# Optimization experiments

Measured on AMD Instinct MI355X. Metric: run time of the kernel, lower is better.

Reference implementation:

```python
import jax, jax.numpy as jnp
import numpy as np

B, C, T = 256, 1, 16384   # batch, input_channels, seq_len
H = C                      # hidden_size == input_channels in this module
OUT = 1                    # output_channels


def setup_inputs() -> dict:
    key = jax.random.key(0)
    ks = jax.random.split(key, 11)
    # PyTorch GRU/Linear init: uniform(-1/sqrt(H), 1/sqrt(H)); H=1 -> (-1, 1)
    u = lambda k, shape, s=1.0: jax.random.uniform(k, shape, jnp.float32, -s, s)
    s_lin = 1.0 / np.sqrt(2 * H).astype(np.float32)
    return {
        "x": jax.random.normal(ks[0], (B, C, T), jnp.float32),
        # layer 0: input size C, per direction [3H, C] / [3H, H] / [3H]
        "w_ih0": u(ks[1], (2, 3 * H, C)),
        "w_hh0": u(ks[2], (2, 3 * H, H)),
        "b_ih0": u(ks[3], (2, 3 * H)),
        "b_hh0": u(ks[4], (2, 3 * H)),
        # layers 1-2: input size 2H (bidirectional concat)
        "w_ih12": u(ks[5], (2, 2, 3 * H, 2 * H)),
        "w_hh12": u(ks[6], (2, 2, 3 * H, H)),
        "b_ih12": u(ks[7], (2, 2, 3 * H)),
        "b_hh12": u(ks[8], (2, 2, 3 * H)),
        # output projection Linear(2H -> OUT)
        "w_out": u(ks[9], (OUT, 2 * H), s_lin),
        "b_out": u(ks[10], (OUT,), s_lin),
    }


def _gru_dir(xs, w_ih, w_hh, b_ih, b_hh, reverse):
    """One GRU direction. xs: [T, B, in] -> ys: [T, B, H] (time-aligned)."""
    h0 = jnp.zeros((xs.shape[1], w_hh.shape[1]), xs.dtype)

    def step(h, x_t):
        gi = x_t @ w_ih.T + b_ih          # [B, 3H]
        gh = h @ w_hh.T + b_hh            # [B, 3H]
        ir, iz, inn = jnp.split(gi, 3, axis=-1)
        hr, hz, hn = jnp.split(gh, 3, axis=-1)
        r = jax.nn.sigmoid(ir + hr)
        z = jax.nn.sigmoid(iz + hz)
        n = jnp.tanh(inn + r * hn)
        h_new = (1.0 - z) * n + z * h
        return h_new, h_new

    _, ys = jax.lax.scan(step, h0, xs, reverse=reverse)
    return ys


def _bidir(xs, w_ih_f, w_hh_f, b_ih_f, b_hh_f, w_ih_b, w_hh_b, b_ih_b, b_hh_b):
    fwd = _gru_dir(xs, w_ih_f, w_hh_f, b_ih_f, b_hh_f, reverse=False)
    bwd = _gru_dir(xs, w_ih_b, w_hh_b, b_ih_b, b_hh_b, reverse=True)
    return jnp.concatenate([fwd, bwd], axis=-1)  # [T, B, 2H]


def reference(x, w_ih0, w_hh0, b_ih0, b_hh0, w_ih12, w_hh12, b_ih12, b_hh12, w_out, b_out):
    xs = jnp.transpose(x, (2, 0, 1))  # [B, C, T] -> [T, B, C]
    xs = _bidir(xs, w_ih0[0], w_hh0[0], b_ih0[0], b_hh0[0],
                w_ih0[1], w_hh0[1], b_ih0[1], b_hh0[1])
    for l in range(2):  # GRU layers 1 and 2 (structurally distinct weights)
        xs = _bidir(xs, w_ih12[l, 0], w_hh12[l, 0], b_ih12[l, 0], b_hh12[l, 0],
                    w_ih12[l, 1], w_hh12[l, 1], b_ih12[l, 1], b_hh12[l, 1])
    y = xs @ w_out.T + b_out          # [T, B, OUT]
    return jnp.transpose(y, (1, 2, 0))  # [B, OUT, T]
```

## Files before the change

kernel.cpp:

```cpp
#include <hip/hip_runtime.h>
#include <hip/hip_fp16.h>

#define T_LEN 16384
#define B_SZ  256
#define S_CH  256
#define CL    (T_LEN / S_CH)
#define HALO  32
#define SC    16

__device__ __forceinline__ float ex2(float x)  { return __builtin_amdgcn_exp2f(x); }
__device__ __forceinline__ float rcpf(float x) { return __builtin_amdgcn_rcpf(x); }

__device__ __forceinline__ float ld_cvt(const float* p)  { return *p; }
__device__ __forceinline__ float ld_cvt(const __half* p) { return __half2float(*p); }
__device__ __forceinline__ void  st_cvt(float* p, float v)  { *p = v; }
__device__ __forceinline__ void  st_cvt(__half* p, float v) { *p = __float2half_rn(v); }

__device__ __forceinline__ float gru_step(float h, float preR, float preZ, float preN,
                                          float UR, float UZ, float UN2, float DN2)
{
    float er  = ex2(fmaf(h, UR, preR));
    float ez  = ex2(fmaf(h, UZ, preZ));
    float r   = rcpf(1.0f + er);
    float z   = rcpf(1.0f + ez);
    float hn2 = fmaf(h, UN2, DN2);
    float en  = ex2(fmaf(r, hn2, preN));
    float n   = fmaf(-2.0f, rcpf(1.0f + en), 1.0f);
    float omz = 1.0f - z;
    float zh  = z * h;
    return fmaf(n, omz, zh);
}

template<bool REV>
__device__ void scan0(const float* __restrict__ x,
                      const float* __restrict__ wih, const float* __restrict__ whh,
                      const float* __restrict__ bih, const float* __restrict__ bhh,
                      __half* __restrict__ out, int b, int s)
{
    const int d = REV ? 1 : 0;
    const float L2E = 1.4426950408889634f;
    const float WR  = -L2E * wih[d*3+0];
    const float WZ  = -L2E * wih[d*3+1];
    const float WN  =  2.0f*L2E * wih[d*3+2];
    const float UR  = -L2E * whh[d*3+0];
    const float UZ  = -L2E * whh[d*3+1];
    const float UN2 =  2.0f*L2E * whh[d*3+2];
    const float CR  = -L2E * (bih[d*3+0] + bhh[d*3+0]);
    const float CZ  = -L2E * (bih[d*3+1] + bhh[d*3+1]);
    const float CN  =  2.0f*L2E * bih[d*3+2];
    const float DN2 =  2.0f*L2E * bhh[d*3+2];

    const int warm   = min(HALO, REV ? (T_LEN - (s + 1) * CL) : (s * CL));
    const int nsteps = warm + CL;
    const int t0     = REV ? ((s + 1) * CL - 1 + warm) : (s * CL - warm);

    const float* row = x + (size_t)b * T_LEN;
    __half* po = out + (REV ? B_SZ : 0) + b;

    float xA[SC], xB[SC];
    float h = 0.0f;

    auto LD = [&](float* F, int base) {
        const float4* p = (const float4*)(row + (REV ? (t0 - base - 15) : (t0 + base)));
        float4 v0 = p[0], v1 = p[1], v2 = p[2], v3 = p[3];
        float lin[16] = { v0.x,v0.y,v0.z,v0.w, v1.x,v1.y,v1.z,v1.w,
                          v2.x,v2.y,v2.z,v2.w, v3.x,v3.y,v3.z,v3.w };
        #pragma unroll
        for (int k = 0; k < 16; ++k) F[k] = REV ? lin[15 - k] : lin[k];
        __builtin_amdgcn_sched_barrier(0);
    };

    auto CS = [&](float* F, int base) {
        float ov[SC];
        #pragma unroll
        for (int k = 0; k < SC; ++k) {
            float xv = F[k];
            h = gru_step(h, fmaf(xv, WR, CR), fmaf(xv, WZ, CZ), fmaf(xv, WN, CN),
                         UR, UZ, UN2, DN2);
            ov[k] = h;
        }
        if (base >= warm) {
            #pragma unroll
            for (int k = 0; k < SC; ++k) {
                int t = REV ? (t0 - (base + k)) : (t0 + (base + k));
                st_cvt(po + t * (2 * B_SZ), ov[k]);
            }
        }
    };

    LD(xA, 0);
    const int nsup = nsteps / SC;
    for (int i = 0; i < nsup; i += 2) {
        LD(xB, min((i + 1) * SC, nsteps - SC));
        CS(xA, i * SC);
        LD(xA, min((i + 2) * SC, nsteps - SC));
        CS(xB, (i + 1) * SC);
    }
}

template<bool REV, typename TIN, typename TOUT>
__device__ void scan12(const TIN* __restrict__ in,
                       const float* __restrict__ wih, const float* __restrict__ whh,
                       const float* __restrict__ bih, const float* __restrict__ bhh,
                       TOUT* __restrict__ out, int b, int s)
{
    const int d = REV ? 1 : 0;
    const float L2E = 1.4426950408889634f;
    const float WR0 = -L2E * wih[(d*3+0)*2+0], WR1 = -L2E * wih[(d*3+0)*2+1];
    const float WZ0 = -L2E * wih[(d*3+1)*2+0], WZ1 = -L2E * wih[(d*3+1)*2+1];
    const float WN0 =  2.0f*L2E * wih[(d*3+2)*2+0], WN1 = 2.0f*L2E * wih[(d*3+2)*2+1];
    const float UR  = -L2E * whh[d*3+0];
    const float UZ  = -L2E * whh[d*3+1];
    const float UN2 =  2.0f*L2E * whh[d*3+2];
    const float CR  = -L2E * (bih[d*3+0] + bhh[d*3+0]);
    const float CZ  = -L2E * (bih[d*3+1] + bhh[d*3+1]);
    const float CN  =  2.0f*L2E * bih[d*3+2];
    const float DN2 =  2.0f*L2E * bhh[d*3+2];

    const int warm   = min(HALO, REV ? (T_LEN - (s + 1) * CL) : (s * CL));
    const int nsteps = warm + CL;
    const int t0     = REV ? ((s + 1) * CL - 1 + warm) : (s * CL - warm);

    const TIN* pf = in + b;
    const TIN* pg = in + B_SZ + b;
    TOUT* po = out + (REV ? B_SZ : 0) + b;

    float fA[SC], gA[SC], fB[SC], gB[SC];
    float h = 0.0f;

#define LD12(F, G, base_) { int base = (base_); \
    _Pragma("unroll") for (int k = 0; k < SC; ++k) { \
      int t = REV ? (t0 - (base + k)) : (t0 + (base + k)); \
      F[k] = ld_cvt(pf + t * (2 * B_SZ)); G[k] = ld_cvt(pg + t * (2 * B_SZ)); } \
    __builtin_amdgcn_sched_barrier(0); }

#define CS12(F, G, base_) { int base = (base_); float ov[SC]; \
    _Pragma("unroll") for (int k = 0; k < SC; ++k) { \
      float a = F[k], c = G[k]; \
      float pr = fmaf(a, WR0, fmaf(c, WR1, CR)); \
      float pz = fmaf(a, WZ0, fmaf(c, WZ1, CZ)); \
      float pn = fmaf(a, WN0, fmaf(c, WN1, CN)); \
      h = gru_step(h, pr, pz, pn, UR, UZ, UN2, DN2); ov[k] = h; } \
    if (base >= warm) { \
      _Pragma("unroll") for (int k = 0; k < SC; ++k) { \
        int t = REV ? (t0 - (base + k)) : (t0 + (base + k)); \
        st_cvt(po + t * (2 * B_SZ), ov[k]); } } }

    LD12(fA, gA, 0);
    const int nsup = nsteps / SC;
    for (int i = 0; i < nsup; i += 2) {
        LD12(fB, gB, min((i + 1) * SC, nsteps - SC));
        CS12(fA, gA, i * SC);
        LD12(fA, gA, min((i + 2) * SC, nsteps - SC));
        CS12(fB, gB, (i + 1) * SC);
    }
#undef LD12
#undef CS12
}

__device__ __forceinline__ void decode_blk(int blk, int tid, int& b, int& s, int& dir)
{
    int xcd = blk & 7;
    int j   = blk >> 3;
    int sl  = j & 31;
    int bg  = (j >> 5) & 3;
    dir     = j >> 7;
    s       = xcd * 32 + sl;
    b       = bg * 64 + tid;
}

__global__ void __launch_bounds__(64) k_scan0g(const float* __restrict__ x,
                                               const float* __restrict__ wih,
                                               const float* __restrict__ whh,
                                               const float* __restrict__ bih,
                                               const float* __restrict__ bhh,
                                               __half* __restrict__ out)
{
    int b, s, dir;
    decode_blk(blockIdx.x, threadIdx.x, b, s, dir);
    if (dir == 0) scan0<false>(x, wih, whh, bih, bhh, out, b, s);
    else          scan0<true >(x, wih, whh, bih, bhh, out, b, s);
}

__global__ void __launch_bounds__(64) k_scan1g(const __half* __restrict__ in,
                                               const float* __restrict__ wih,
                                               const float* __restrict__ whh,
                                               const float* __restrict__ bih,
                                               const float* __restrict__ bhh,
                                               __half* __restrict__ out)
{
    int b, s, dir;
    decode_blk(blockIdx.x, threadIdx.x, b, s, dir);
    if (dir == 0) scan12<false>(in, wih, whh, bih, bhh, out, b, s);
    else          scan12<true >(in, wih, whh, bih, bhh, out, b, s);
}

__global__ void __launch_bounds__(64) k_scan2g(const __half* __restrict__ in,
                                               const float* __restrict__ wih,
                                               const float* __restrict__ whh,
                                               const float* __restrict__ bih,
                                               const float* __restrict__ bhh,
                                               float* __restrict__ out)
{
    int b, s, dir;
    decode_blk(blockIdx.x, threadIdx.x, b, s, dir);
    if (dir == 0) scan12<false>(in, wih, whh, bih, bhh, out, b, s);
    else          scan12<true >(in, wih, whh, bih, bhh, out, b, s);
}

__global__ void __launch_bounds__(256) k_proj(const float* __restrict__ h2,
                                              const float* __restrict__ wo,
                                              const float* __restrict__ bo,
                                              float* __restrict__ y)
{
    __shared__ float tile[64][65];
    const int b0 = (blockIdx.x & 3) * 64;
    const int t0 = (blockIdx.x >> 2) * 64;
    const float wf = wo[0], wb = wo[1], bias = bo[0];
    const int bl = threadIdx.x & 63;
    const int tg = threadIdx.x >> 6;
    #pragma unroll
    for (int i = 0; i < 16; ++i) {
        int tl = tg * 16 + i;
        int t  = t0 + tl;
        float f = h2[(size_t)t * (2 * B_SZ) + b0 + bl];
        float g = h2[(size_t)t * (2 * B_SZ) + B_SZ + b0 + bl];
        tile[bl][tl] = fmaf(wf, f, fmaf(wb, g, bias));
    }
    __syncthreads();
    const int c4 = threadIdx.x & 15;
    const int r  = threadIdx.x >> 4;
    #pragma unroll
    for (int i = 0; i < 4; ++i) {
        int brow = r + 16 * i;
        float4 v = make_float4(tile[brow][c4*4+0], tile[brow][c4*4+1],
                               tile[brow][c4*4+2], tile[brow][c4*4+3]);
        ((float4*)y)[(size_t)(b0 + brow) * (T_LEN / 4) + t0 / 4 + c4] = v;
    }
}

extern "C" void kernel_launch(void* const* d_in, const int* in_sizes, int n_in,
                              void* d_out, int out_size, void* d_ws, size_t ws_size,
                              hipStream_t stream)
{
    (void)in_sizes; (void)n_in; (void)out_size; (void)ws_size;
    const float* x      = (const float*)d_in[0];
    const float* w_ih0  = (const float*)d_in[1];
    const float* w_hh0  = (const float*)d_in[2];
    const float* b_ih0  = (const float*)d_in[3];
    const float* b_hh0  = (const float*)d_in[4];
    const float* w_ih12 = (const float*)d_in[5];
    const float* w_hh12 = (const float*)d_in[6];
    const float* b_ih12 = (const float*)d_in[7];
    const float* b_hh12 = (const float*)d_in[8];
    const float* w_out  = (const float*)d_in[9];
    const float* b_out  = (const float*)d_in[10];
    float* y = (float*)d_out;

    char* ws = (char*)d_ws;
    const size_t NN = (size_t)2 * B_SZ * T_LEN;
    __half* l0out = (__half*)ws;
    __half* l1out = (__half*)(ws + NN * 2);
    float*  l2out = (float*)(ws + NN * 4);

    const int nblk = 8 * S_CH;
    k_scan0g<<<nblk, 64, 0, stream>>>(x,     w_ih0,       w_hh0,      b_ih0,      b_hh0,      l0out);
    k_scan1g<<<nblk, 64, 0, stream>>>(l0out, w_ih12 + 0,  w_hh12 + 0, b_ih12 + 0, b_hh12 + 0, l1out);
    k_scan2g<<<nblk, 64, 0, stream>>>(l1out, w_ih12 + 12, w_hh12 + 6, b_ih12 + 6, b_hh12 + 6, l2out);
    k_proj  <<<1024, 256, 0, stream>>>(l2out, w_out, b_out, y);
}
```

Measured before the change: 136.5 us.

## Fuse last GRU layer's two directions with output projection in one kernel

```diff
diff --git a/kernel.cpp b/kernel.cpp
--- a/kernel.cpp
+++ b/kernel.cpp
@@ -98,11 +98,11 @@
     }
 }
 
-template<bool REV, typename TIN, typename TOUT>
-__device__ void scan12(const TIN* __restrict__ in,
-                       const float* __restrict__ wih, const float* __restrict__ whh,
-                       const float* __restrict__ bih, const float* __restrict__ bhh,
-                       TOUT* __restrict__ out, int b, int s)
+template<bool REV>
+__device__ void scan1(const __half* __restrict__ in,
+                      const float* __restrict__ wih, const float* __restrict__ whh,
+                      const float* __restrict__ bih, const float* __restrict__ bhh,
+                      __half* __restrict__ out, int b, int s)
 {
     const int d = REV ? 1 : 0;
     const float L2E = 1.4426950408889634f;
@@ -121,9 +121,9 @@
     const int nsteps = warm + CL;
     const int t0     = REV ? ((s + 1) * CL - 1 + warm) : (s * CL - warm);
 
-    const TIN* pf = in + b;
-    const TIN* pg = in + B_SZ + b;
-    TOUT* po = out + (REV ? B_SZ : 0) + b;
+    const __half* pf = in + b;
+    const __half* pg = in + B_SZ + b;
+    __half* po = out + (REV ? B_SZ : 0) + b;
 
     float fA[SC], gA[SC], fB[SC], gB[SC];
     float h = 0.0f;
@@ -158,6 +158,129 @@
 #undef CS12
 }
 
+template<bool S0, bool SLAST>
+__device__ void scan2p(const __half* __restrict__ in,
+                       const float* __restrict__ wih, const float* __restrict__ whh,
+                       const float* __restrict__ bih, const float* __restrict__ bhh,
+                       const float* __restrict__ wo,  const float* __restrict__ bo,
+                       float* __restrict__ y, int b, int s)
+{
+    const float L2E = 1.4426950408889634f;
+    const float WR0f = -L2E*wih[0], WR1f = -L2E*wih[1];
+    const float WZ0f = -L2E*wih[2], WZ1f = -L2E*wih[3];
+    const float WN0f = 2.0f*L2E*wih[4], WN1f = 2.0f*L2E*wih[5];
+    const float URf  = -L2E*whh[0], UZf = -L2E*whh[1], UN2f = 2.0f*L2E*whh[2];
+    const float CRf  = -L2E*(bih[0]+bhh[0]), CZf = -L2E*(bih[1]+bhh[1]);
+    const float CNf  = 2.0f*L2E*bih[2], DN2f = 2.0f*L2E*bhh[2];
+    const float WR0b = -L2E*wih[6],  WR1b = -L2E*wih[7];
+    const float WZ0b = -L2E*wih[8],  WZ1b = -L2E*wih[9];
+    const float WN0b = 2.0f*L2E*wih[10], WN1b = 2.0f*L2E*wih[11];
+    const float URb  = -L2E*whh[3], UZb = -L2E*whh[4], UN2b = 2.0f*L2E*whh[5];
+    const float CRb  = -L2E*(bih[3]+bhh[3]), CZb = -L2E*(bih[4]+bhh[4]);
+    const float CNb  = 2.0f*L2E*bih[5], DN2b = 2.0f*L2E*bhh[5];
+    const float wf = wo[0], wbk = wo[1], bias = bo[0];
+
+    const __half* pf = in + b;
+    const __half* pg = in + B_SZ + b;
+
+    float fA[SC], gA[SC], fB[SC], gB[SC];
+    float hf[CL];
+    float h;
+
+    constexpr int warmf = S0 ? 0 : HALO;
+    const int t0f = s * CL - warmf;
+
+#define LDF(F, G, base) { \
+    _Pragma("unroll") for (int k = 0; k < SC; ++k) { \
+      int t = t0f + (base) + k; \
+      F[k] = __half2float(pf[t * (2 * B_SZ)]); G[k] = __half2float(pg[t * (2 * B_SZ)]); } \
+    __builtin_amdgcn_sched_barrier(0); }
+#define STEPF(F, G, k) { float a = F[k], c = G[k]; \
+    float pr = fmaf(a, WR0f, fmaf(c, WR1f, CRf)); \
+    float pz = fmaf(a, WZ0f, fmaf(c, WZ1f, CZf)); \
+    float pn = fmaf(a, WN0f, fmaf(c, WN1f, CNf)); \
+    h = gru_step(h, pr, pz, pn, URf, UZf, UN2f, DN2f); }
+#define CSF_B(F, G) { _Pragma("unroll") for (int k = 0; k < SC; ++k) { STEPF(F, G, k); } }
+#define CSF_S(F, G, off) { _Pragma("unroll") for (int k = 0; k < SC; ++k) { STEPF(F, G, k); hf[(off)+k] = h; } }
+
+    h = 0.0f;
+    LDF(fA, gA, 0);
+    LDF(fB, gB, 16);
+    if constexpr (!S0) {
+        CSF_B(fA, gA);
+        LDF(fA, gA, 32);
+        CSF_B(fB, gB);
+        LDF(fB, gB, 48);
+        CSF_S(fA, gA, 0);
+        LDF(fA, gA, 64);
+        CSF_S(fB, gB, 16);
+        LDF(fB, gB, 80);
+        CSF_S(fA, gA, 32);
+        CSF_S(fB, gB, 48);
+    } else {
+        CSF_S(fA, gA, 0);
+        LDF(fA, gA, 32);
+        CSF_S(fB, gB, 16);
+        LDF(fB, gB, 48);
+        CSF_S(fA, gA, 32);
+        CSF_S(fB, gB, 48);
+    }
+#undef LDF
+#undef STEPF
+#undef CSF_B
+#undef CSF_S
+
+    constexpr int warmb = SLAST ? 0 : HALO;
+    const int t0b = (s + 1) * CL - 1 + warmb;
+    float yv[CL];
+
+#define LDB(F, G, base) { \
+    _Pragma("unroll") for (int k = 0; k < SC; ++k) { \
+      int t = t0b - ((base) + k); \
+      F[k] = __half2float(pf[t * (2 * B_SZ)]); G[k] = __half2float(pg[t * (2 * B_SZ)]); } \
+    __builtin_amdgcn_sched_barrier(0); }
+#define STEPB(F, G, k) { float a = F[k], c = G[k]; \
+    float pr = fmaf(a, WR0b, fmaf(c, WR1b, CRb)); \
+    float pz = fmaf(a, WZ0b, fmaf(c, WZ1b, CZb)); \
+    float pn = fmaf(a, WN0b, fmaf(c, WN1b, CNb)); \
+    h = gru_step(h, pr, pz, pn, URb, UZb, UN2b, DN2b); }
+#define CSB_B(F, G) { _Pragma("unroll") for (int k = 0; k < SC; ++k) { STEPB(F, G, k); } }
+#define CSB_S(F, G, off) { _Pragma("unroll") for (int k = 0; k < SC; ++k) { STEPB(F, G, k); \
+    yv[(off)-k] = fmaf(wf, hf[(off)-k], fmaf(wbk, h, bias)); } }
+
+    h = 0.0f;
+    LDB(fA, gA, 0);
+    LDB(fB, gB, 16);
+    if constexpr (!SLAST) {
+        CSB_B(fA, gA);
+        LDB(fA, gA, 32);
+        CSB_B(fB, gB);
+        LDB(fB, gB, 48);
+        CSB_S(fA, gA, 63);
+        LDB(fA, gA, 64);
+        CSB_S(fB, gB, 47);
+        LDB(fB, gB, 80);
+        CSB_S(fA, gA, 31);
+        CSB_S(fB, gB, 15);
+    } else {
+        CSB_S(fA, gA, 63);
+        LDB(fA, gA, 32);
+        CSB_S(fB, gB, 47);
+        LDB(fB, gB, 48);
+        CSB_S(fA, gA, 31);
+        CSB_S(fB, gB, 15);
+    }
+#undef LDB
+#undef STEPB
+#undef CSB_B
+#undef CSB_S
+
+    float4* yp = (float4*)(y + (size_t)b * T_LEN + s * CL);
+    #pragma unroll
+    for (int i = 0; i < 16; ++i)
+        yp[i] = make_float4(yv[4*i], yv[4*i+1], yv[4*i+2], yv[4*i+3]);
+}
+
 __device__ __forceinline__ void decode_blk(int blk, int tid, int& b, int& s, int& dir)
 {
     int xcd = blk & 7;
@@ -191,52 +314,28 @@
 {
     int b, s, dir;
     decode_blk(blockIdx.x, threadIdx.x, b, s, dir);
-    if (dir == 0) scan12<false>(in, wih, whh, bih, bhh, out, b, s);
-    else          scan12<true >(in, wih, whh, bih, bhh, out, b, s);
-}
-
-__global__ void __launch_bounds__(64) k_scan2g(const __half* __restrict__ in,
+    if (dir == 0) scan1<false>(in, wih, whh, bih, bhh, out, b, s);
+    else          scan1<true >(in, wih, whh, bih, bhh, out, b, s);
+}
+
+__global__ void __launch_bounds__(64) k_scan2p(const __half* __restrict__ in,
                                                const float* __restrict__ wih,
                                                const float* __restrict__ whh,
                                                const float* __restrict__ bih,
                                                const float* __restrict__ bhh,
-                                               float* __restrict__ out)
-{
-    int b, s, dir;
-    decode_blk(blockIdx.x, threadIdx.x, b, s, dir);
-    if (dir == 0) scan12<false>(in, wih, whh, bih, bhh, out, b, s);
-    else          scan12<true >(in, wih, whh, bih, bhh, out, b, s);
-}
-
-__global__ void __launch_bounds__(256) k_proj(const float* __restrict__ h2,
-                                              const float* __restrict__ wo,
-                                              const float* __restrict__ bo,
-                                              float* __restrict__ y)
-{
-    __shared__ float tile[64][65];
-    const int b0 = (blockIdx.x & 3) * 64;
-    const int t0 = (blockIdx.x >> 2) * 64;
-    const float wf = wo[0], wb = wo[1], bias = bo[0];
-    const int bl = threadIdx.x & 63;
-    const int tg = threadIdx.x >> 6;
-    #pragma unroll
-    for (int i = 0; i < 16; ++i) {
-        int tl = tg * 16 + i;
-        int t  = t0 + tl;
-        float f = h2[(size_t)t * (2 * B_SZ) + b0 + bl];
-        float g = h2[(size_t)t * (2 * B_SZ) + B_SZ + b0 + bl];
-        tile[bl][tl] = fmaf(wf, f, fmaf(wb, g, bias));
-    }
-    __syncthreads();
-    const int c4 = threadIdx.x & 15;
-    const int r  = threadIdx.x >> 4;
-    #pragma unroll
-    for (int i = 0; i < 4; ++i) {
-        int brow = r + 16 * i;
-        float4 v = make_float4(tile[brow][c4*4+0], tile[brow][c4*4+1],
-                               tile[brow][c4*4+2], tile[brow][c4*4+3]);
-        ((float4*)y)[(size_t)(b0 + brow) * (T_LEN / 4) + t0 / 4 + c4] = v;
-    }
+                                               const float* __restrict__ wo,
+                                               const float* __restrict__ bo,
+                                               float* __restrict__ y)
+{
+    int xcd = blockIdx.x & 7;
+    int j   = blockIdx.x >> 3;
+    int sl  = j & 31;
+    int bg  = j >> 5;
+    int s   = xcd * 32 + sl;
+    int b   = bg * 64 + threadIdx.x;
+    if (s == 0)               scan2p<true,  false>(in, wih, whh, bih, bhh, wo, bo, y, b, s);
+    else if (s == S_CH - 1)   scan2p<false, true >(in, wih, whh, bih, bhh, wo, bo, y, b, s);
+    else                      scan2p<false, false>(in, wih, whh, bih, bhh, wo, bo, y, b, s);
 }
 
 extern "C" void kernel_launch(void* const* d_in, const int* in_sizes, int n_in,
@@ -261,11 +360,9 @@
     const size_t NN = (size_t)2 * B_SZ * T_LEN;
     __half* l0out = (__half*)ws;
     __half* l1out = (__half*)(ws + NN * 2);
-    float*  l2out = (float*)(ws + NN * 4);
-
-    const int nblk = 8 * S_CH;
-    k_scan0g<<<nblk, 64, 0, stream>>>(x,     w_ih0,       w_hh0,      b_ih0,      b_hh0,      l0out);
-    k_scan1g<<<nblk, 64, 0, stream>>>(l0out, w_ih12 + 0,  w_hh12 + 0, b_ih12 + 0, b_hh12 + 0, l1out);
-    k_scan2g<<<nblk, 64, 0, stream>>>(l1out, w_ih12 + 12, w_hh12 + 6, b_ih12 + 6, b_hh12 + 6, l2out);
-    k_proj  <<<1024, 256, 0, stream>>>(l2out, w_out, b_out, y);
-}
+
+    k_scan0g<<<2048, 64, 0, stream>>>(x,     w_ih0,       w_hh0,      b_ih0,      b_hh0,      l0out);
+    k_scan1g<<<2048, 64, 0, stream>>>(l0out, w_ih12 + 0,  w_hh12 + 0, b_ih12 + 0, b_hh12 + 0, l1out);
+    k_scan2p<<<1024, 64, 0, stream>>>(l1out, w_ih12 + 12, w_hh12 + 6, b_ih12 + 6, b_hh12 + 6,
+                                      w_out, b_out, y);
+}
```

New measurement: 143.2 us. 1.05x slower.
